# Kernel tuning notes

Hardware: AMD Instinct MI355X
Metric: run time of the kernel (lower is better)

## Reference

```python
import jax, jax.numpy as jnp
import numpy as np

T, F_IN, UNITS, N_CLASSES = 21, 126, 8, 27


def _run_lstm(seq, Wk, Wr, b):
    """Keras-style LSTM (gate order i,f,g,o). seq: (B,T,F) -> hs: (B,T,U)."""
    B = seq.shape[0]
    U = Wr.shape[0]
    # input projection for all timesteps at once: (B,T,4U)
    z_in = jnp.einsum('btf,fg->btg', seq, Wk) + b

    def step(carry, z_t):
        h, c = carry
        z = z_t + h @ Wr
        i, f, g, o = jnp.split(z, 4, axis=-1)
        i = jax.nn.sigmoid(i)
        f = jax.nn.sigmoid(f)
        g = jnp.tanh(g)
        o = jax.nn.sigmoid(o)
        c = f * c + i * g
        h = o * jnp.tanh(c)
        return (h, c), h

    h0 = jnp.zeros((B, U), seq.dtype)
    (_, _), hs = jax.lax.scan(step, (h0, h0), jnp.swapaxes(z_in, 0, 1))
    return jnp.swapaxes(hs, 0, 1)  # (B,T,U)


def setup_inputs() -> dict:
    key = jax.random.key(0)
    ks = jax.random.split(key, 6)
    B = 32768
    return {
        'x': jax.random.normal(ks[0], (B, T * F_IN), dtype=jnp.float32),
        'W1k': jax.random.normal(ks[1], (F_IN, 4 * UNITS), dtype=jnp.float32) * 0.1,
        'W1r': jax.random.normal(ks[2], (UNITS, 4 * UNITS), dtype=jnp.float32) * 0.1,
        'b1': jnp.zeros((4 * UNITS,), jnp.float32),
        'W2k': jax.random.normal(ks[3], (UNITS, 4 * UNITS), dtype=jnp.float32) * 0.1,
        'W2r': jax.random.normal(ks[4], (UNITS, 4 * UNITS), dtype=jnp.float32) * 0.1,
        'b2': jnp.zeros((4 * UNITS,), jnp.float32),
        'Wd': jax.random.normal(ks[5], (UNITS, N_CLASSES), dtype=jnp.float32) * 0.1,
        'bd': jnp.zeros((N_CLASSES,), jnp.float32),
    }


def reference(x, W1k, W1r, b1, W2k, W2r, b2, Wd, bd):
    B = x.shape[0]
    seq = x.reshape(B, T, F_IN)            # Reshape((21, 126))
    h1 = _run_lstm(seq, W1k, W1r, b1)      # LSTM(8, return_sequences=True)
    # dropout is identity at inference
    h2 = _run_lstm(h1, W2k, W2r, b2)[:, -1]  # LSTM(8) -> last step (B,8)
    return jax.nn.softmax(h2 @ Wd + bd)    # Dense(27, softmax)
```

## Files before the change

### kernel.cpp

```cpp
#include <hip/hip_runtime.h>


namespace {
constexpr int T_  = 21;
constexpr int FIN = 126;
constexpr int U_  = 8;
constexpr int NC  = 27;
constexpr int ZC  = 4 * U_;
constexpr int ROW = T_ * FIN;
}

__device__ __forceinline__ float sigm(float x) {
  return __builtin_amdgcn_rcpf(1.0f + __expf(-x));
}
__device__ __forceinline__ float tanh_f(float x) {
  return 1.0f - 2.0f * __builtin_amdgcn_rcpf(1.0f + __expf(2.0f * x));
}

__global__ __launch_bounds__(256) void lstm_fused(
    const float* __restrict__ X,
    const float* __restrict__ W1k, const float* __restrict__ b1,
    const float* __restrict__ W1r,
    const float* __restrict__ W2k, const float* __restrict__ W2r,
    const float* __restrict__ b2,
    const float* __restrict__ Wd, const float* __restrict__ bd,
    float* __restrict__ out)
{
  __shared__ __align__(16) float xb[2][64 * FIN];
  __shared__ __align__(16) float zb1[ZC * 64];
  __shared__ __align__(16) float zb2[ZC * 64];

  const int tid = threadIdx.x;
  const int sl  = tid & 63;
  const int wv  = __builtin_amdgcn_readfirstlane(tid >> 6);
  const int grp = blockIdx.x;

  int  goff[16];
  int  loff[16];
  bool val[16];
  #pragma unroll
  for (int k = 0; k < 16; ++k) {
    int j = tid + k * 256;
    val[k] = (j < 64 * 63);
    int s = j / 63;
    int q = j - s * 63;
    goff[k] = s * ROW + 2 * q;
    loff[k] = s * FIN + 2 * q;
  }

  const float* xbase = X + (size_t)grp * 64 * ROW;

  const float4* Wk4 = reinterpret_cast<const float4*>(W1k) + 2 * wv;
  const float4  b1a = reinterpret_cast<const float4*>(b1)[2 * wv];
  const float4  b1b = reinterpret_cast<const float4*>(b1)[2 * wv + 1];
  const float4  b2a = reinterpret_cast<const float4*>(b2)[2 * wv];
  const float4  b2b = reinterpret_cast<const float4*>(b2)[2 * wv + 1];

  float h1[U_], c1[U_], h2[U_], c2[U_];
  #pragma unroll
  for (int u = 0; u < U_; ++u) { h1[u] = 0.f; c1[u] = 0.f; h2[u] = 0.f; c2[u] = 0.f; }

  float2 pf[16];
  #pragma unroll
  for (int k = 0; k < 16; ++k)
    if (val[k]) pf[k] = *reinterpret_cast<const float2*>(xbase + goff[k]);

  int p = 0;
  for (int t = 0; t < T_; ++t) {
    #pragma unroll
    for (int k = 0; k < 16; ++k)
      if (val[k]) *reinterpret_cast<float2*>(&xb[p][loff[k]]) = pf[k];
    __syncthreads();

    if (t + 1 < T_) {
      const float* xt = xbase + (t + 1) * FIN;
      #pragma unroll
      for (int k = 0; k < 16; ++k)
        if (val[k]) pf[k] = *reinterpret_cast<const float2*>(xt + goff[k]);
    }

    float4 za = b1a, zbv = b1b;
    const float2* xr = reinterpret_cast<const float2*>(&xb[p][sl * FIN]);
    #pragma unroll 3
    for (int q = 0; q < 63; ++q) {
      float2 xv = xr[q];
      float4 wa0 = Wk4[(2 * q) * 8];
      float4 wb0 = Wk4[(2 * q) * 8 + 1];
      float4 wa1 = Wk4[(2 * q + 1) * 8];
      float4 wb1 = Wk4[(2 * q + 1) * 8 + 1];
      za.x  = fmaf(xv.x, wa0.x, za.x);  za.y  = fmaf(xv.x, wa0.y, za.y);
      za.z  = fmaf(xv.x, wa0.z, za.z);  za.w  = fmaf(xv.x, wa0.w, za.w);
      zbv.x = fmaf(xv.x, wb0.x, zbv.x); zbv.y = fmaf(xv.x, wb0.y, zbv.y);
      zbv.z = fmaf(xv.x, wb0.z, zbv.z); zbv.w = fmaf(xv.x, wb0.w, zbv.w);
      za.x  = fmaf(xv.y, wa1.x, za.x);  za.y  = fmaf(xv.y, wa1.y, za.y);
      za.z  = fmaf(xv.y, wa1.z, za.z);  za.w  = fmaf(xv.y, wa1.w, za.w);
      zbv.x = fmaf(xv.y, wb1.x, zbv.x); zbv.y = fmaf(xv.y, wb1.y, zbv.y);
      zbv.z = fmaf(xv.y, wb1.z, zbv.z); zbv.w = fmaf(xv.y, wb1.w, zbv.w);
    }

    #pragma unroll
    for (int k = 0; k < U_; ++k) {
      float hv = h1[k];
      const float* w = &W1r[k * ZC + 8 * wv];
      za.x  = fmaf(hv, w[0], za.x);  za.y  = fmaf(hv, w[1], za.y);
      za.z  = fmaf(hv, w[2], za.z);  za.w  = fmaf(hv, w[3], za.w);
      zbv.x = fmaf(hv, w[4], zbv.x); zbv.y = fmaf(hv, w[5], zbv.y);
      zbv.z = fmaf(hv, w[6], zbv.z); zbv.w = fmaf(hv, w[7], zbv.w);
    }

    {
      float* zp = &zb1[(8 * wv) * 64 + sl];
      zp[0 * 64] = za.x;  zp[1 * 64] = za.y;  zp[2 * 64] = za.z;  zp[3 * 64] = za.w;
      zp[4 * 64] = zbv.x; zp[5 * 64] = zbv.y; zp[6 * 64] = zbv.z; zp[7 * 64] = zbv.w;
    }
    __syncthreads();

    #pragma unroll
    for (int u = 0; u < U_; ++u) {
      float zi = zb1[u * 64 + sl];
      float zf = zb1[(U_ + u) * 64 + sl];
      float zg = zb1[(2 * U_ + u) * 64 + sl];
      float zo = zb1[(3 * U_ + u) * 64 + sl];
      float iv = sigm(zi), fv = sigm(zf), gv = tanh_f(zg), ov = sigm(zo);
      float cn = fv * c1[u] + iv * gv;
      c1[u] = cn;
      h1[u] = ov * tanh_f(cn);
    }

    {
      float4 za2 = b2a, zb2v = b2b;
      #pragma unroll
      for (int k = 0; k < U_; ++k) {
        float hv = h1[k];
        const float* w = &W2k[k * ZC + 8 * wv];
        za2.x  = fmaf(hv, w[0], za2.x);  za2.y  = fmaf(hv, w[1], za2.y);
        za2.z  = fmaf(hv, w[2], za2.z);  za2.w  = fmaf(hv, w[3], za2.w);
        zb2v.x = fmaf(hv, w[4], zb2v.x); zb2v.y = fmaf(hv, w[5], zb2v.y);
        zb2v.z = fmaf(hv, w[6], zb2v.z); zb2v.w = fmaf(hv, w[7], zb2v.w);
      }
      #pragma unroll
      for (int k = 0; k < U_; ++k) {
        float hv = h2[k];
        const float* w = &W2r[k * ZC + 8 * wv];
        za2.x  = fmaf(hv, w[0], za2.x);  za2.y  = fmaf(hv, w[1], za2.y);
        za2.z  = fmaf(hv, w[2], za2.z);  za2.w  = fmaf(hv, w[3], za2.w);
        zb2v.x = fmaf(hv, w[4], zb2v.x); zb2v.y = fmaf(hv, w[5], zb2v.y);
        zb2v.z = fmaf(hv, w[6], zb2v.z); zb2v.w = fmaf(hv, w[7], zb2v.w);
      }
      float* zp = &zb2[(8 * wv) * 64 + sl];
      zp[0 * 64] = za2.x;  zp[1 * 64] = za2.y;  zp[2 * 64] = za2.z;  zp[3 * 64] = za2.w;
      zp[4 * 64] = zb2v.x; zp[5 * 64] = zb2v.y; zp[6 * 64] = zb2v.z; zp[7 * 64] = zb2v.w;
    }
    __syncthreads();

    #pragma unroll
    for (int u = 0; u < U_; ++u) {
      float zi = zb2[u * 64 + sl];
      float zf = zb2[(U_ + u) * 64 + sl];
      float zg = zb2[(2 * U_ + u) * 64 + sl];
      float zo = zb2[(3 * U_ + u) * 64 + sl];
      float iv = sigm(zi), fv = sigm(zf), gv = tanh_f(zg), ov = sigm(zo);
      float cn = fv * c2[u] + iv * gv;
      c2[u] = cn;
      h2[u] = ov * tanh_f(cn);
    }

    p ^= 1;
  }

  float lg[NC];
  float m = -1e30f;
  #pragma unroll
  for (int c = 0; c < NC; ++c) {
    float acc = bd[c];
    #pragma unroll
    for (int k = 0; k < U_; ++k) acc = fmaf(h2[k], Wd[k * NC + c], acc);
    lg[c] = acc;
    m = fmaxf(m, acc);
  }
  float ssum = 0.f;
  #pragma unroll
  for (int c = 0; c < NC; ++c) {
    float e = __expf(lg[c] - m);
    lg[c] = e;
    ssum += e;
  }
  float inv = 1.0f / ssum;
  if (wv == 0) {
    #pragma unroll
    for (int c = 0; c < NC; ++c) zb1[sl * NC + c] = lg[c] * inv;
  }
  __syncthreads();
  {
    float* oblk = out + (size_t)grp * 64 * NC;
    #pragma unroll
    for (int k = 0; k < 7; ++k) {
      int j = tid + k * 256;
      if (j < 64 * NC) oblk[j] = zb1[j];
    }
  }
}

extern "C" void kernel_launch(void* const* d_in, const int* in_sizes, int n_in,
                              void* d_out, int out_size, void* d_ws, size_t ws_size,
                              hipStream_t stream) {
  const float* X   = (const float*)d_in[0];
  const float* W1k = (const float*)d_in[1];
  const float* W1r = (const float*)d_in[2];
  const float* b1  = (const float*)d_in[3];
  const float* W2k = (const float*)d_in[4];
  const float* W2r = (const float*)d_in[5];
  const float* b2  = (const float*)d_in[6];
  const float* Wd  = (const float*)d_in[7];
  const float* bd  = (const float*)d_in[8];
  float* out = (float*)d_out;
  (void)d_ws; (void)ws_size;

  const int B    = in_sizes[0] / ROW;
  const int ngrp = B / 64;

  lstm_fused<<<dim3(ngrp), 256, 0, stream>>>(
      X, W1k, b1, W1r, W2k, W2r, b2, Wd, bd, out);
}
```

Measured before the change: 550.3 us.

## Split input projection across two wave halves and specialize recurrent state per layer

Result: faster. 526.1 us (-4.4%).

```diff
diff --git a/kernel.cpp b/kernel.cpp
--- a/kernel.cpp
+++ b/kernel.cpp
@@ -8,6 +8,8 @@
 constexpr int NC  = 27;
 constexpr int ZC  = 4 * U_;
 constexpr int ROW = T_ * FIN;
+constexpr int NT  = 512;
+constexpr int NPF = 8;
 }
 
 __device__ __forceinline__ float sigm(float x) {
@@ -17,7 +19,7 @@
   return 1.0f - 2.0f * __builtin_amdgcn_rcpf(1.0f + __expf(2.0f * x));
 }
 
-__global__ __launch_bounds__(256) void lstm_fused(
+__global__ __launch_bounds__(NT) void lstm_fused(
     const float* __restrict__ X,
     const float* __restrict__ W1k, const float* __restrict__ b1,
     const float* __restrict__ W1r,
@@ -26,21 +28,23 @@
     const float* __restrict__ Wd, const float* __restrict__ bd,
     float* __restrict__ out)
 {
-  __shared__ __align__(16) float xb[2][64 * FIN];
-  __shared__ __align__(16) float zb1[ZC * 64];
-  __shared__ __align__(16) float zb2[ZC * 64];
+  __shared__ __align__(16) float xb[64 * FIN];
+  __shared__ __align__(16) float zb1[ZC * 2 * 64];
+  __shared__ __align__(16) float zb2[ZC * 2 * 64];
 
   const int tid = threadIdx.x;
   const int sl  = tid & 63;
   const int wv  = __builtin_amdgcn_readfirstlane(tid >> 6);
+  const int cg  = wv & 3;
+  const int fh  = wv >> 2;
   const int grp = blockIdx.x;
 
-  int  goff[16];
-  int  loff[16];
-  bool val[16];
-  #pragma unroll
-  for (int k = 0; k < 16; ++k) {
-    int j = tid + k * 256;
+  int  goff[NPF];
+  int  loff[NPF];
+  bool val[NPF];
+  #pragma unroll
+  for (int k = 0; k < NPF; ++k) {
+    int j = tid + k * NT;
     val[k] = (j < 64 * 63);
     int s = j / 63;
     int q = j - s * 63;
@@ -50,143 +54,173 @@
 
   const float* xbase = X + (size_t)grp * 64 * ROW;
 
-  const float4* Wk4 = reinterpret_cast<const float4*>(W1k) + 2 * wv;
-  const float4  b1a = reinterpret_cast<const float4*>(b1)[2 * wv];
-  const float4  b1b = reinterpret_cast<const float4*>(b1)[2 * wv + 1];
-  const float4  b2a = reinterpret_cast<const float4*>(b2)[2 * wv];
-  const float4  b2b = reinterpret_cast<const float4*>(b2)[2 * wv + 1];
-
-  float h1[U_], c1[U_], h2[U_], c2[U_];
-  #pragma unroll
-  for (int u = 0; u < U_; ++u) { h1[u] = 0.f; c1[u] = 0.f; h2[u] = 0.f; c2[u] = 0.f; }
-
-  float2 pf[16];
-  #pragma unroll
-  for (int k = 0; k < 16; ++k)
+  const float4* Wk4 = reinterpret_cast<const float4*>(W1k) + 2 * cg;
+  const float*  Wrr = (fh == 0) ? W1r : W2r;
+  const float4  b1a = reinterpret_cast<const float4*>(b1)[2 * cg];
+  const float4  b1b = reinterpret_cast<const float4*>(b1)[2 * cg + 1];
+  const float4  b2a = reinterpret_cast<const float4*>(b2)[2 * cg];
+  const float4  b2b = reinterpret_cast<const float4*>(b2)[2 * cg + 1];
+
+  float hs[U_], cs[U_];
+  #pragma unroll
+  for (int u = 0; u < U_; ++u) { hs[u] = 0.f; cs[u] = 0.f; }
+
+  float2 pf[NPF];
+  #pragma unroll
+  for (int k = 0; k < NPF; ++k)
     if (val[k]) pf[k] = *reinterpret_cast<const float2*>(xbase + goff[k]);
-
-  int p = 0;
+  #pragma unroll
+  for (int k = 0; k < NPF; ++k)
+    if (val[k]) *reinterpret_cast<float2*>(&xb[loff[k]]) = pf[k];
+  {
+    const float* xt = xbase + FIN;
+    #pragma unroll
+    for (int k = 0; k < NPF; ++k)
+      if (val[k]) pf[k] = *reinterpret_cast<const float2*>(xt + goff[k]);
+  }
+  __syncthreads();
+
   for (int t = 0; t < T_; ++t) {
-    #pragma unroll
-    for (int k = 0; k < 16; ++k)
-      if (val[k]) *reinterpret_cast<float2*>(&xb[p][loff[k]]) = pf[k];
+    float4 za, zbv;
+    if (fh == 0) { za = b1a; zbv = b1b; }
+    else {
+      za  = make_float4(0.f, 0.f, 0.f, 0.f);
+      zbv = make_float4(0.f, 0.f, 0.f, 0.f);
+    }
+
+    const float2* xr = reinterpret_cast<const float2*>(&xb[sl * FIN]);
+    auto run_gemm = [&](const int q0, const int qn) {
+      #pragma unroll 4
+      for (int qq = 0; qq < qn; ++qq) {
+        const int q = q0 + qq;
+        float2 xv  = xr[q];
+        float4 wa0 = Wk4[(2 * q) * 8];
+        float4 wb0 = Wk4[(2 * q) * 8 + 1];
+        float4 wa1 = Wk4[(2 * q + 1) * 8];
+        float4 wb1 = Wk4[(2 * q + 1) * 8 + 1];
+        za.x  = fmaf(xv.x, wa0.x, za.x);  za.y  = fmaf(xv.x, wa0.y, za.y);
+        za.z  = fmaf(xv.x, wa0.z, za.z);  za.w  = fmaf(xv.x, wa0.w, za.w);
+        zbv.x = fmaf(xv.x, wb0.x, zbv.x); zbv.y = fmaf(xv.x, wb0.y, zbv.y);
+        zbv.z = fmaf(xv.x, wb0.z, zbv.z); zbv.w = fmaf(xv.x, wb0.w, zbv.w);
+        za.x  = fmaf(xv.y, wa1.x, za.x);  za.y  = fmaf(xv.y, wa1.y, za.y);
+        za.z  = fmaf(xv.y, wa1.z, za.z);  za.w  = fmaf(xv.y, wa1.w, za.w);
+        zbv.x = fmaf(xv.y, wb1.x, zbv.x); zbv.y = fmaf(xv.y, wb1.y, zbv.y);
+        zbv.z = fmaf(xv.y, wb1.z, zbv.z); zbv.w = fmaf(xv.y, wb1.w, zbv.w);
+      }
+    };
+    if (fh == 0) run_gemm(0, 32);
+    else         run_gemm(32, 31);
+
+    if (fh == 0) {
+      #pragma unroll
+      for (int k = 0; k < U_; ++k) {
+        float hv = hs[k];
+        const float* w = &Wrr[k * ZC + 8 * cg];
+        za.x  = fmaf(hv, w[0], za.x);  za.y  = fmaf(hv, w[1], za.y);
+        za.z  = fmaf(hv, w[2], za.z);  za.w  = fmaf(hv, w[3], za.w);
+        zbv.x = fmaf(hv, w[4], zbv.x); zbv.y = fmaf(hv, w[5], zbv.y);
+        zbv.z = fmaf(hv, w[6], zbv.z); zbv.w = fmaf(hv, w[7], zbv.w);
+      }
+    }
+
+    {
+      float* zp = &zb1[(8 * cg) * 128 + fh * 64 + sl];
+      zp[0 * 128] = za.x;  zp[1 * 128] = za.y;  zp[2 * 128] = za.z;  zp[3 * 128] = za.w;
+      zp[4 * 128] = zbv.x; zp[5 * 128] = zbv.y; zp[6 * 128] = zbv.z; zp[7 * 128] = zbv.w;
+    }
     __syncthreads();
 
     if (t + 1 < T_) {
-      const float* xt = xbase + (t + 1) * FIN;
-      #pragma unroll
-      for (int k = 0; k < 16; ++k)
+      #pragma unroll
+      for (int k = 0; k < NPF; ++k)
+        if (val[k]) *reinterpret_cast<float2*>(&xb[loff[k]]) = pf[k];
+    }
+    if (t + 2 < T_) {
+      const float* xt = xbase + (size_t)(t + 2) * FIN;
+      #pragma unroll
+      for (int k = 0; k < NPF; ++k)
         if (val[k]) pf[k] = *reinterpret_cast<const float2*>(xt + goff[k]);
     }
 
-    float4 za = b1a, zbv = b1b;
-    const float2* xr = reinterpret_cast<const float2*>(&xb[p][sl * FIN]);
-    #pragma unroll 3
-    for (int q = 0; q < 63; ++q) {
-      float2 xv = xr[q];
-      float4 wa0 = Wk4[(2 * q) * 8];
-      float4 wb0 = Wk4[(2 * q) * 8 + 1];
-      float4 wa1 = Wk4[(2 * q + 1) * 8];
-      float4 wb1 = Wk4[(2 * q + 1) * 8 + 1];
-      za.x  = fmaf(xv.x, wa0.x, za.x);  za.y  = fmaf(xv.x, wa0.y, za.y);
-      za.z  = fmaf(xv.x, wa0.z, za.z);  za.w  = fmaf(xv.x, wa0.w, za.w);
-      zbv.x = fmaf(xv.x, wb0.x, zbv.x); zbv.y = fmaf(xv.x, wb0.y, zbv.y);
-      zbv.z = fmaf(xv.x, wb0.z, zbv.z); zbv.w = fmaf(xv.x, wb0.w, zbv.w);
-      za.x  = fmaf(xv.y, wa1.x, za.x);  za.y  = fmaf(xv.y, wa1.y, za.y);
-      za.z  = fmaf(xv.y, wa1.z, za.z);  za.w  = fmaf(xv.y, wa1.w, za.w);
-      zbv.x = fmaf(xv.y, wb1.x, zbv.x); zbv.y = fmaf(xv.y, wb1.y, zbv.y);
-      zbv.z = fmaf(xv.y, wb1.z, zbv.z); zbv.w = fmaf(xv.y, wb1.w, zbv.w);
-    }
-
-    #pragma unroll
-    for (int k = 0; k < U_; ++k) {
-      float hv = h1[k];
-      const float* w = &W1r[k * ZC + 8 * wv];
-      za.x  = fmaf(hv, w[0], za.x);  za.y  = fmaf(hv, w[1], za.y);
-      za.z  = fmaf(hv, w[2], za.z);  za.w  = fmaf(hv, w[3], za.w);
-      zbv.x = fmaf(hv, w[4], zbv.x); zbv.y = fmaf(hv, w[5], zbv.y);
-      zbv.z = fmaf(hv, w[6], zbv.z); zbv.w = fmaf(hv, w[7], zbv.w);
-    }
-
-    {
-      float* zp = &zb1[(8 * wv) * 64 + sl];
-      zp[0 * 64] = za.x;  zp[1 * 64] = za.y;  zp[2 * 64] = za.z;  zp[3 * 64] = za.w;
-      zp[4 * 64] = zbv.x; zp[5 * 64] = zbv.y; zp[6 * 64] = zbv.z; zp[7 * 64] = zbv.w;
-    }
-    __syncthreads();
-
-    #pragma unroll
-    for (int u = 0; u < U_; ++u) {
-      float zi = zb1[u * 64 + sl];
-      float zf = zb1[(U_ + u) * 64 + sl];
-      float zg = zb1[(2 * U_ + u) * 64 + sl];
-      float zo = zb1[(3 * U_ + u) * 64 + sl];
-      float iv = sigm(zi), fv = sigm(zf), gv = tanh_f(zg), ov = sigm(zo);
-      float cn = fv * c1[u] + iv * gv;
-      c1[u] = cn;
-      h1[u] = ov * tanh_f(cn);
-    }
-
-    {
+    if (fh == 0) {
+      #pragma unroll
+      for (int u = 0; u < U_; ++u) {
+        const float* p0 = &zb1[u * 128 + sl];
+        float zi = p0[0]            + p0[64];
+        float zf = p0[ 8 * 128]     + p0[ 8 * 128 + 64];
+        float zg = p0[16 * 128]     + p0[16 * 128 + 64];
+        float zo = p0[24 * 128]     + p0[24 * 128 + 64];
+        float iv = sigm(zi), fv = sigm(zf), gv = tanh_f(zg), ov = sigm(zo);
+        float cn = fv * cs[u] + iv * gv;
+        cs[u] = cn;
+        hs[u] = ov * tanh_f(cn);
+      }
       float4 za2 = b2a, zb2v = b2b;
       #pragma unroll
       for (int k = 0; k < U_; ++k) {
-        float hv = h1[k];
-        const float* w = &W2k[k * ZC + 8 * wv];
+        float hv = hs[k];
+        const float* w = &W2k[k * ZC + 8 * cg];
         za2.x  = fmaf(hv, w[0], za2.x);  za2.y  = fmaf(hv, w[1], za2.y);
         za2.z  = fmaf(hv, w[2], za2.z);  za2.w  = fmaf(hv, w[3], za2.w);
         zb2v.x = fmaf(hv, w[4], zb2v.x); zb2v.y = fmaf(hv, w[5], zb2v.y);
         zb2v.z = fmaf(hv, w[6], zb2v.z); zb2v.w = fmaf(hv, w[7], zb2v.w);
       }
+      float* zp = &zb2[(8 * cg) * 128 + 0 * 64 + sl];
+      zp[0 * 128] = za2.x;  zp[1 * 128] = za2.y;  zp[2 * 128] = za2.z;  zp[3 * 128] = za2.w;
+      zp[4 * 128] = zb2v.x; zp[5 * 128] = zb2v.y; zp[6 * 128] = zb2v.z; zp[7 * 128] = zb2v.w;
+    } else {
+      float4 za2  = make_float4(0.f, 0.f, 0.f, 0.f);
+      float4 zb2v = make_float4(0.f, 0.f, 0.f, 0.f);
       #pragma unroll
       for (int k = 0; k < U_; ++k) {
-        float hv = h2[k];
-        const float* w = &W2r[k * ZC + 8 * wv];
+        float hv = hs[k];
+        const float* w = &Wrr[k * ZC + 8 * cg];
         za2.x  = fmaf(hv, w[0], za2.x);  za2.y  = fmaf(hv, w[1], za2.y);
         za2.z  = fmaf(hv, w[2], za2.z);  za2.w  = fmaf(hv, w[3], za2.w);
         zb2v.x = fmaf(hv, w[4], zb2v.x); zb2v.y = fmaf(hv, w[5], zb2v.y);
         zb2v.z = fmaf(hv, w[6], zb2v.z); zb2v.w = fmaf(hv, w[7], zb2v.w);
       }
-      float* zp = &zb2[(8 * wv) * 64 + sl];
-      zp[0 * 64] = za2.x;  zp[1 * 64] = za2.y;  zp[2 * 64] = za2.z;  zp[3 * 64] = za2.w;
-      zp[4 * 64] = zb2v.x; zp[5 * 64] = zb2v.y; zp[6 * 64] = zb2v.z; zp[7 * 64] = zb2v.w;
+      float* zp = &zb2[(8 * cg) * 128 + 1 * 64 + sl];
+      zp[0 * 128] = za2.x;  zp[1 * 128] = za2.y;  zp[2 * 128] = za2.z;  zp[3 * 128] = za2.w;
+      zp[4 * 128] = zb2v.x; zp[5 * 128] = zb2v.y; zp[6 * 128] = zb2v.z; zp[7 * 128] = zb2v.w;
     }
     __syncthreads();
 
-    #pragma unroll
-    for (int u = 0; u < U_; ++u) {
-      float zi = zb2[u * 64 + sl];
-      float zf = zb2[(U_ + u) * 64 + sl];
-      float zg = zb2[(2 * U_ + u) * 64 + sl];
-      float zo = zb2[(3 * U_ + u) * 64 + sl];
-      float iv = sigm(zi), fv = sigm(zf), gv = tanh_f(zg), ov = sigm(zo);
-      float cn = fv * c2[u] + iv * gv;
-      c2[u] = cn;
-      h2[u] = ov * tanh_f(cn);
-    }
-
-    p ^= 1;
-  }
-
-  float lg[NC];
-  float m = -1e30f;
-  #pragma unroll
-  for (int c = 0; c < NC; ++c) {
-    float acc = bd[c];
-    #pragma unroll
-    for (int k = 0; k < U_; ++k) acc = fmaf(h2[k], Wd[k * NC + c], acc);
-    lg[c] = acc;
-    m = fmaxf(m, acc);
-  }
-  float ssum = 0.f;
-  #pragma unroll
-  for (int c = 0; c < NC; ++c) {
-    float e = __expf(lg[c] - m);
-    lg[c] = e;
-    ssum += e;
-  }
-  float inv = 1.0f / ssum;
-  if (wv == 0) {
+    if (fh == 1) {
+      #pragma unroll
+      for (int u = 0; u < U_; ++u) {
+        const float* p0 = &zb2[u * 128 + sl];
+        float zi = p0[0]            + p0[64];
+        float zf = p0[ 8 * 128]     + p0[ 8 * 128 + 64];
+        float zg = p0[16 * 128]     + p0[16 * 128 + 64];
+        float zo = p0[24 * 128]     + p0[24 * 128 + 64];
+        float iv = sigm(zi), fv = sigm(zf), gv = tanh_f(zg), ov = sigm(zo);
+        float cn = fv * cs[u] + iv * gv;
+        cs[u] = cn;
+        hs[u] = ov * tanh_f(cn);
+      }
+    }
+  }
+
+  if (wv == 4) {
+    float lg[NC];
+    float m = -1e30f;
+    #pragma unroll
+    for (int c = 0; c < NC; ++c) {
+      float acc = bd[c];
+      #pragma unroll
+      for (int k = 0; k < U_; ++k) acc = fmaf(hs[k], Wd[k * NC + c], acc);
+      lg[c] = acc;
+      m = fmaxf(m, acc);
+    }
+    float ssum = 0.f;
+    #pragma unroll
+    for (int c = 0; c < NC; ++c) {
+      float e = __expf(lg[c] - m);
+      lg[c] = e;
+      ssum += e;
+    }
+    float inv = 1.0f / ssum;
     #pragma unroll
     for (int c = 0; c < NC; ++c) zb1[sl * NC + c] = lg[c] * inv;
   }
@@ -194,8 +228,8 @@
   {
     float* oblk = out + (size_t)grp * 64 * NC;
     #pragma unroll
-    for (int k = 0; k < 7; ++k) {
-      int j = tid + k * 256;
+    for (int k = 0; k < 4; ++k) {
+      int j = tid + k * NT;
       if (j < 64 * NC) oblk[j] = zb1[j];
     }
   }
@@ -219,6 +253,6 @@
   const int B    = in_sizes[0] / ROW;
   const int ngrp = B / 64;
 
-  lstm_fused<<<dim3(ngrp), 256, 0, stream>>>(
+  lstm_fused<<<dim3(ngrp), NT, 0, stream>>>(
       X, W1k, b1, W1r, W2k, W2r, b2, Wd, bd, out);
 }
```
